# Kernel tuning notes

Hardware: AMD Instinct MI355X
Metric: run time of the kernel (lower is better)

Reference implementation:

```python
import jax, jax.numpy as jnp
import numpy as np

L, N, E, D, H = 3, 20000, 320000, 128, 4
EPS = 1.1920929e-07  # torch RMSNorm default eps = finfo(float32).eps
NEG_SLOPE = 0.2      # PyG GATConv leaky_relu negative_slope


def rmsnorm(x, w):
    return x * jax.lax.rsqrt(jnp.mean(x * x, axis=-1, keepdims=True) + EPS) * w


def setup_inputs() -> dict:
    key = jax.random.key(0)
    ks = jax.random.split(key, 13)
    s = 0.02
    x = jax.random.normal(ks[0], (N, D), jnp.float32)
    src = jax.random.randint(ks[1], (E,), 0, N, dtype=jnp.int64)
    dst = jax.random.randint(ks[2], (E,), 0, N, dtype=jnp.int64)
    dst = jnp.where(dst == src, (dst + 1) % N, dst)  # no pre-existing self loops
    edge_index = jnp.stack([src, dst])
    return {
        "x": x,
        "W_gat": jax.random.normal(ks[3], (L, D, H * D), jnp.float32) * s,
        "att_src": jax.random.normal(ks[4], (L, H, D), jnp.float32) * s,
        "att_dst": jax.random.normal(ks[5], (L, H, D), jnp.float32) * s,
        "bias_gat": jax.random.normal(ks[6], (L, D), jnp.float32) * s,
        "W1": jax.random.normal(ks[7], (L, D, D), jnp.float32) * s,
        "b1": jax.random.normal(ks[8], (L, D), jnp.float32) * s,
        "W2": jax.random.normal(ks[9], (L, D, D), jnp.float32) * s,
        "b2": jax.random.normal(ks[10], (L, D), jnp.float32) * s,
        "norm1_w": jnp.ones((L, D), jnp.float32),
        "norm2_w": jnp.ones((L, D), jnp.float32),
        "edge_index": edge_index,
    }


def reference(x, W_gat, att_src, att_dst, bias_gat, W1, b1, W2, b2, norm1_w, norm2_w, edge_index):
    # PyG GATConv adds self loops by default
    loops = jnp.arange(N, dtype=edge_index.dtype)
    src = jnp.concatenate([edge_index[0], loops])  # [E+N]
    dst = jnp.concatenate([edge_index[1], loops])
    for i in range(L):
        # --- GATConv(hidden, hidden, heads=H, concat=False), dropout=0 (eval) ---
        xp = (x @ W_gat[i]).reshape(N, H, D)               # [N,H,D]
        a_s = jnp.einsum('nhd,hd->nh', xp, att_src[i])     # [N,H]
        a_d = jnp.einsum('nhd,hd->nh', xp, att_dst[i])
        e = jax.nn.leaky_relu(a_s[src] + a_d[dst], NEG_SLOPE)  # [E+N,H]
        m = jax.ops.segment_max(e, dst, num_segments=N)
        ex = jnp.exp(e - m[dst])
        denom = jax.ops.segment_sum(ex, dst, num_segments=N)
        alpha = ex / denom[dst]                             # segment softmax over incoming edges
        agg = jax.ops.segment_sum(alpha[:, :, None] * xp[src], dst, num_segments=N)  # [N,H,D]
        x_att = agg.mean(axis=1) + bias_gat[i]              # concat=False -> head mean, then bias
        # --- residual + RMSNorm ---
        x = rmsnorm(x + x_att, norm1_w[i])
        # --- FFN ---
        h = jax.nn.relu(x @ W1[i] + b1[i])
        h = h @ W2[i] + b2[i]
        x = rmsnorm(x + h, norm2_w[i])
    return x
```

## Files before the change

kernel.cpp:

```cpp
#include <hip/hip_runtime.h>
#include <hip/hip_bf16.h>

#define N_NODES 20000
#define NEDGE   320000
#define DIM     128
#define NH      4
#define HD      512
#define LAYERS  3
#define EPS_RMS 1.1920929e-07f
#define SLOPE   0.2f
#define NTILES  (N_NODES >> 4)

#define NWGC  (LAYERS * DIM * HD)
#define NW1C  (LAYERS * DIM * DIM)
#define NVC   (LAYERS * DIM)
#define NPACK (NWGC + 2 * NW1C + 5 * NVC)
#define NXV   (N_NODES * DIM / 8)

typedef __bf16 bf16_t;
typedef __bf16 bf16v2 __attribute__((ext_vector_type(2)));
typedef __bf16 bf16v8 __attribute__((ext_vector_type(8)));
typedef float  f32v4  __attribute__((ext_vector_type(4)));
typedef float  f32v2  __attribute__((ext_vector_type(2)));

__device__ __forceinline__ int clamp_node(int s) {
    return ((unsigned)s >= (unsigned)N_NODES) ? 0 : s;
}
__device__ __forceinline__ float leaky(float e) { return e > 0.f ? e : SLOPE * e; }
__device__ __forceinline__ unsigned char enc_fp8(float v) {
    int p = __builtin_amdgcn_cvt_pk_fp8_f32(v, v, 0, false);
    return (unsigned char)(p & 0xff);
}
__device__ __forceinline__ unsigned short enc_fp8_pair(float a, float b) {
    int p = __builtin_amdgcn_cvt_pk_fp8_f32(a, b, 0, false);
    return (unsigned short)(p & 0xffff);
}

__device__ __forceinline__ bool wave_detect_bf16(const unsigned short* xh) {
    int lane = threadIdx.x & 63;
    unsigned short hw = xh[2 * lane];
    int e = (hw >> 7) & 0xff;
    unsigned long long b = __ballot(e >= 96 && e <= 140);
    return __popcll(b) >= 48;
}
__device__ __forceinline__ bool wave_detect_i64(const int* ei) {
    int lane = threadIdx.x & 63;
    unsigned long long b = __ballot(ei[2 * lane + 1] != 0);
    return b == 0ULL;
}
__device__ __forceinline__ float raw_elem(const void* in, size_t j, bool isbf) {
    return isbf ? (float)((const bf16_t*)in)[j] : ((const float*)in)[j];
}
__device__ __forceinline__ bf16_t cvt_elem(const void* in, size_t j, bool isbf) {
    return isbf ? ((const bf16_t*)in)[j] : (bf16_t)((const float*)in)[j];
}
__device__ __forceinline__ int edge_src(const int* ei, int e, bool is64) {
    return clamp_node(is64 ? ei[2 * e] : ei[e]);
}
__device__ __forceinline__ int edge_dst(const int* ei, int e, bool is64) {
    return clamp_node(is64 ? ei[2 * NEDGE + 2 * e] : ei[NEDGE + e]);
}

__global__ __launch_bounds__(256) void prep_v(const void* x, const void* Wg,
                                              const void* aS, const void* aD,
                                              float* __restrict__ vS, float* __restrict__ vD,
                                              int* __restrict__ deg) {
    int gid = blockIdx.x * 256 + threadIdx.x;
    for (int i = gid; i < N_NODES; i += gridDim.x * 256) deg[i] = 0;
    bool isbf = wave_detect_bf16((const unsigned short*)x);
    int w = gid >> 6;
    if (w >= LAYERS * DIM * NH * 2) return;
    int lane = threadIdx.x & 63;
    int sd = w & 1, h = (w >> 1) & 3, k = (w >> 3) & 127, l = w >> 10;
    const void* att = sd ? aD : aS;
    size_t wbase = (size_t)l * DIM * HD + (size_t)k * HD + h * DIM;
    size_t abase = (size_t)l * NH * DIM + (size_t)h * DIM;
    int c = 2 * lane;
    float p = raw_elem(Wg, wbase + c, isbf) * raw_elem(att, abase + c, isbf)
            + raw_elem(Wg, wbase + c + 1, isbf) * raw_elem(att, abase + c + 1, isbf);
#pragma unroll
    for (int msk = 1; msk < 64; msk <<= 1) p += __shfl_xor(p, msk);
    if (lane == 0) {
        float* dst = sd ? vD : vS;
        dst[l * HD + h * DIM + k] = p;
    }
}

__device__ __forceinline__ void pack_item(int i, bool isbf,
        const void* Wg, const void* W1, const void* W2,
        const void* bg, const void* b1, const void* b2,
        const void* n1, const void* n2,
        bf16_t* WmixP, bf16_t* W1P, bf16_t* W2P,
        bf16_t* bgc, bf16_t* b1c, bf16_t* b2c, bf16_t* n1c, bf16_t* n2c) {
    if (i < NWGC) {
        int l = i >> 16;
        int r = i & 65535;
        int j = r & 7;
        int lane2 = (r >> 3) & 63;
        int mm = lane2 & 15, kqq = lane2 >> 4;
        int tt = (r >> 9) & 1;
        int kk = (r >> 10) & 15;
        int wvv = r >> 14;
        int kidx = kk * 32 + kqq * 8 + j;
        int h = kidx >> 7, kp = kidx & 127;
        int c = 32 * wvv + tt * 16 + mm;
        WmixP[i] = cvt_elem(Wg, (size_t)l * DIM * HD + (size_t)kp * HD + h * DIM + c, isbf);
        return;
    }
    i -= NWGC;
    if (i < NW1C) {
        int l = i / 16384;
        int r = i & 16383;
        int j = r & 7;
        int lane2 = (r >> 3) & 63;
        int mm = lane2 & 15, kqq = lane2 >> 4;
        int tt = (r >> 9) & 1;
        int ks = (r >> 10) & 3;
        int wvv = r >> 12;
        int k = ks * 32 + kqq * 8 + j;
        int c = 32 * wvv + tt * 16 + mm;
        W1P[i] = cvt_elem(W1, (size_t)l * DIM * DIM + (size_t)k * DIM + c, isbf);
        return;
    }
    i -= NW1C;
    if (i < NW1C) {
        int l = i / 16384;
        int r = i & 16383;
        int j = r & 7;
        int lane2 = (r >> 3) & 63;
        int mm = lane2 & 15, kqq = lane2 >> 4;
        int tt = (r >> 9) & 1;
        int ks = (r >> 10) & 3;
        int wvv = r >> 12;
        int k = ks * 32 + kqq * 8 + j;
        int c = 32 * wvv + tt * 16 + mm;
        W2P[i] = cvt_elem(W2, (size_t)l * DIM * DIM + (size_t)k * DIM + c, isbf);
        return;
    }
    i -= NW1C;
    if (i >= 5 * NVC) return;
    int seg = i / NVC, k = i - seg * NVC;
    if (seg == 0) bgc[k] = cvt_elem(bg, k, isbf);
    else if (seg == 1) b1c[k] = cvt_elem(b1, k, isbf);
    else if (seg == 2) b2c[k] = cvt_elem(b2, k, isbf);
    else if (seg == 3) n1c[k] = cvt_elem(n1, k, isbf);
    else n2c[k] = cvt_elem(n2, k, isbf);
}

__global__ __launch_bounds__(256) void mega_setup(
        const void* x, const void* Wg, const void* W1, const void* W2,
        const void* bg, const void* b1, const void* b2, const void* n1, const void* n2,
        bf16_t* xb, bf16_t* WmixP, bf16_t* W1P, bf16_t* W2P,
        bf16_t* bgc, bf16_t* b1c, bf16_t* b2c, bf16_t* n1c, bf16_t* n2c,
        const int* ei, int* deg,
        const float* vS, const float* vD,
        float* a_s, float* a_d, unsigned short* x8,
        int convBlocks, int histBlocks) {
    int b = (int)blockIdx.x;
    if (b >= convBlocks + histBlocks) {
        bool isbf = wave_detect_bf16((const unsigned short*)x);
        int lane = threadIdx.x & 63;
        int n = (b - convBlocks - histBlocks) * 4 + (int)(threadIdx.x >> 6);
        if (n >= N_NODES) return;
        int c = 2 * lane;
        float f0 = raw_elem(x, (size_t)n * DIM + c, isbf);
        float f1 = raw_elem(x, (size_t)n * DIM + c + 1, isbf);
        x8[n * 64 + lane] = enc_fp8_pair(f0, f1);
#pragma unroll
        for (int h = 0; h < NH; ++h) {
            float ps = f0 * vS[h * DIM + c] + f1 * vS[h * DIM + c + 1];
            float pd = f0 * vD[h * DIM + c] + f1 * vD[h * DIM + c + 1];
#pragma unroll
            for (int msk = 1; msk < 64; msk <<= 1) {
                ps += __shfl_xor(ps, msk);
                pd += __shfl_xor(pd, msk);
            }
            if (lane == 0) {
                a_s[n * 4 + h] = ps;
                a_d[n * 4 + h] = pd;
            }
        }
        return;
    }
    if (b >= convBlocks) {
        bool is64 = wave_detect_i64(ei);
        int e = (b - convBlocks) * 256 + threadIdx.x;
        if (e < NEDGE) atomicAdd(&deg[edge_dst(ei, e, is64)], 1);
        return;
    }
    bool isbf = wave_detect_bf16((const unsigned short*)x);
    int i = b * 256 + threadIdx.x;
    if (i < NXV) {
        if (isbf) {
            ((bf16v8*)xb)[i] = ((const bf16v8*)x)[i];
        } else {
            const float4* src = (const float4*)x;
            float4 a = src[2 * i], bq = src[2 * i + 1];
            bf16v8 o;
            o[0] = (bf16_t)a.x;  o[1] = (bf16_t)a.y;
            o[2] = (bf16_t)a.z;  o[3] = (bf16_t)a.w;
            o[4] = (bf16_t)bq.x; o[5] = (bf16_t)bq.y;
            o[6] = (bf16_t)bq.z; o[7] = (bf16_t)bq.w;
            ((bf16v8*)xb)[i] = o;
        }
        return;
    }
    pack_item(i - NXV, isbf, Wg, W1, W2, bg, b1, b2, n1, n2,
              WmixP, W1P, W2P, bgc, b1c, b2c, n1c, n2c);
}

__global__ __launch_bounds__(1024) void scan_kernel(const int* __restrict__ deg,
                                                    int* __restrict__ row_ptr,
                                                    int* __restrict__ cursor) {
    __shared__ int wsum[16];
    int tid = threadIdx.x, lane = tid & 63, wv = tid >> 6;
    int v[20];
    int base = tid * 20;
    int tot = 0;
    if (base < N_NODES) {
        const int4* d4 = reinterpret_cast<const int4*>(deg + base);
#pragma unroll
        for (int j = 0; j < 5; ++j) {
            int4 q = d4[j];
            v[4 * j]     = q.x;
            v[4 * j + 1] = q.y;
            v[4 * j + 2] = q.z;
            v[4 * j + 3] = q.w;
        }
#pragma unroll
        for (int i = 0; i < 20; ++i) tot += v[i];
    }
    int x = tot;
#pragma unroll
    for (int off = 1; off < 64; off <<= 1) {
        int t = __shfl_up(x, off);
        if (lane >= off) x += t;
    }
    if (lane == 63) wsum[wv] = x;
    __syncthreads();
    if (wv == 0) {
        int s = (lane < 16) ? wsum[lane] : 0;
#pragma unroll
        for (int off = 1; off < 16; off <<= 1) {
            int t = __shfl_up(s, off);
            if (lane >= off) s += t;
        }
        if (lane < 16) wsum[lane] = s;
    }
    __syncthreads();
    int off0 = ((wv == 0) ? 0 : wsum[wv - 1]) + (x - tot);
    if (tid == 0) row_ptr[0] = 0;
    if (base < N_NODES) {
        int run = off0;
#pragma unroll
        for (int i = 0; i < 20; ++i) {
            run += v[i];
            row_ptr[base + i + 1] = run;
            cursor[base + i] = run - v[i];
        }
    }
}

__global__ void fill_kernel(const int* __restrict__ ei, int* __restrict__ cursor,
                            int* __restrict__ csr_src) {
    bool is64 = wave_detect_i64(ei);
    int e = blockIdx.x * blockDim.x + threadIdx.x;
    if (e < NEDGE) {
        int d = edge_dst(ei, e, is64);
        int pos = atomicAdd(&cursor[d], 1);
        if ((unsigned)pos < (unsigned)NEDGE) csr_src[pos] = edge_src(ei, e, is64);
    }
}

__global__ __launch_bounds__(256) void gat_gather(const int* __restrict__ row_ptr,
                                                  const int* __restrict__ csr_src,
                                                  const float* __restrict__ a_s,
                                                  const float* __restrict__ a_d,
                                                  const unsigned short* __restrict__ x8,
                                                  bf16_t* __restrict__ y) {
    __shared__ float4 wsh[4][64];
    __shared__ int    ssh[4][64];
    int n = (int)((blockIdx.x * blockDim.x + threadIdx.x) >> 6);
    if (n >= N_NODES) return;
    int wv = (int)(threadIdx.x >> 6) & 3;
    int lane = threadIdx.x & 63;
    int beg = row_ptr[n];
    int deg = row_ptr[n + 1] - beg;
    if (deg < 0) deg = 0;
    if (deg > NEDGE) deg = NEDGE;
    if (beg < 0) beg = 0;
    if (beg > NEDGE - deg) beg = NEDGE - deg;

    const float4* a_s4 = reinterpret_cast<const float4*>(a_s);
    const float4 adv = reinterpret_cast<const float4*>(a_d)[n];
    const float4 avs = a_s4[n];
    unsigned short pself = x8[n * 64 + lane];
    float4 wself = {__expf(leaky(avs.x + adv.x)), __expf(leaky(avs.y + adv.y)),
                    __expf(leaky(avs.z + adv.z)), __expf(leaky(avs.w + adv.w))};

    float acc[8];
    {
        f32v2 f = __builtin_amdgcn_cvt_pk_f32_fp8((int)pself, false);
        acc[0] = wself.x * f[0]; acc[1] = wself.x * f[1];
        acc[2] = wself.y * f[0]; acc[3] = wself.y * f[1];
        acc[4] = wself.z * f[0]; acc[5] = wself.z * f[1];
        acc[6] = wself.w * f[0]; acc[7] = wself.w * f[1];
    }

    float4 zl = {0.f, 0.f, 0.f, 0.f};
    for (int c0 = 0; c0 < deg; c0 += 64) {
        int cnt = deg - c0; if (cnt > 64) cnt = 64;
        if (lane < cnt) {
            int s = clamp_node(csr_src[beg + c0 + lane]);
            float4 av = a_s4[s];
            float4 w = {__expf(leaky(av.x + adv.x)), __expf(leaky(av.y + adv.y)),
                        __expf(leaky(av.z + adv.z)), __expf(leaky(av.w + adv.w))};
            zl.x += w.x; zl.y += w.y; zl.z += w.z; zl.w += w.w;
            wsh[wv][lane] = w;
            ssh[wv][lane] = s << 6;
        }
        unsigned short xeN[8];
        {
            int p0 = cnt < 8 ? cnt : 8;
#pragma unroll
            for (int u = 0; u < 8; ++u)
                if (u < p0) xeN[u] = x8[ssh[wv][u] + lane];
        }
        for (int u0 = 0; u0 < cnt; u0 += 8) {
            int uc = cnt - u0; if (uc > 8) uc = 8;
            unsigned short xeC[8];
#pragma unroll
            for (int u = 0; u < 8; ++u) xeC[u] = xeN[u];
            int n0 = u0 + 8;
            int nc = cnt - n0; if (nc > 8) nc = 8;
#pragma unroll
            for (int u = 0; u < 8; ++u)
                if (u < nc) xeN[u] = x8[ssh[wv][n0 + u] + lane];
#pragma unroll
            for (int u = 0; u < 8; ++u) {
                if (u < uc) {
                    float4 w = wsh[wv][u0 + u];
                    f32v2 f = __builtin_amdgcn_cvt_pk_f32_fp8((int)xeC[u], false);
                    acc[0] += w.x * f[0]; acc[1] += w.x * f[1];
                    acc[2] += w.y * f[0]; acc[3] += w.y * f[1];
                    acc[4] += w.z * f[0]; acc[5] += w.z * f[1];
                    acc[6] += w.w * f[0]; acc[7] += w.w * f[1];
                }
            }
        }
    }
    float4 zr = zl;
#pragma unroll
    for (int msk = 1; msk < 64; msk <<= 1) {
        zr.x += __shfl_xor(zr.x, msk);
        zr.y += __shfl_xor(zr.y, msk);
        zr.z += __shfl_xor(zr.z, msk);
        zr.w += __shfl_xor(zr.w, msk);
    }
    float4 z4 = {wself.x + zr.x, wself.y + zr.y, wself.z + zr.z, wself.w + zr.w};
    float4 ih4 = {1.f / z4.x, 1.f / z4.y, 1.f / z4.z, 1.f / z4.w};
    int c = 2 * lane;
#pragma unroll
    for (int h = 0; h < NH; ++h) {
        float ih = h == 0 ? ih4.x : h == 1 ? ih4.y : h == 2 ? ih4.z : ih4.w;
        bf16v2 o;
        o[0] = (bf16_t)(acc[h * 2 + 0] * ih);
        o[1] = (bf16_t)(acc[h * 2 + 1] * ih);
        *reinterpret_cast<bf16v2*>(&y[(size_t)n * HD + h * DIM + c]) = o;
    }
}

template <int MODE>
__global__ __launch_bounds__(256) void mix_ffn(
        const bf16_t* __restrict__ y,
        const bf16_t* __restrict__ WmixP, const bf16_t* __restrict__ bg,
        const bf16_t* __restrict__ n1w, const bf16_t* __restrict__ xb,
        const bf16_t* __restrict__ W1P, const bf16_t* __restrict__ b1,
        const bf16_t* __restrict__ W2P, const bf16_t* __restrict__ b2,
        const bf16_t* __restrict__ n2w, void* __restrict__ out,
        const float* __restrict__ vS, const float* __restrict__ vD,
        float* __restrict__ a_s_n, float* __restrict__ a_d_n,
        unsigned char* __restrict__ x8_n) {
    __shared__ bf16_t ylds[16][524];
    __shared__ bf16_t xm[16][140];
    __shared__ float  ssq_p[16][4];
    __shared__ float  asd_p[4][16][8];
    bf16_t (*hh)[140] = reinterpret_cast<bf16_t (*)[140]>(&ylds[0][0]);

    int tile = blockIdx.x;
    int wv = threadIdx.x >> 6;
    int lane = threadIdx.x & 63;
    int m = lane & 15, kq = lane >> 4;

    const bf16_t* ybase = y + (size_t)tile * 16 * HD;
#pragma unroll
    for (int it = 0; it < 8; ++it) {
        int f = it * 2048 + (int)threadIdx.x * 8;
        int row = f >> 9, col = f & 511;
        *reinterpret_cast<bf16v8*>(&ylds[row][col]) =
            *reinterpret_cast<const bf16v8*>(ybase + f);
    }
    __syncthreads();

    f32v4 accm[2];
    accm[0] = (f32v4){0.f, 0.f, 0.f, 0.f};
    accm[1] = (f32v4){0.f, 0.f, 0.f, 0.f};
#pragma unroll
    for (int kk = 0; kk < 16; ++kk) {
        bf16v8 a = *reinterpret_cast<const bf16v8*>(&ylds[m][kk * 32 + kq * 8]);
#pragma unroll
        for (int tt = 0; tt < 2; ++tt) {
            bf16v8 b = *reinterpret_cast<const bf16v8*>(
                WmixP + ((((wv * 16 + kk) * 2 + tt) << 9) + lane * 8));
            accm[tt] = __builtin_amdgcn_mfma_f32_16x16x32_bf16(a, b, accm[tt], 0, 0, 0);
        }
    }
    float vals[2][4];
    {
        float sp[4] = {0.f, 0.f, 0.f, 0.f};
#pragma unroll
        for (int tt = 0; tt < 2; ++tt) {
            int col = 32 * wv + tt * 16 + m;
            float bv = (float)bg[col];
#pragma unroll
            for (int r = 0; r < 4; ++r) {
                int gr = tile * 16 + kq * 4 + r;
                float v = 0.25f * accm[tt][r] + bv + (float)xb[(size_t)gr * DIM + col];
                vals[tt][r] = v;
                sp[r] += v * v;
            }
        }
#pragma unroll
        for (int r = 0; r < 4; ++r) {
            sp[r] += __shfl_xor(sp[r], 1); sp[r] += __shfl_xor(sp[r], 2);
            sp[r] += __shfl_xor(sp[r], 4); sp[r] += __shfl_xor(sp[r], 8);
            if (m == r) ssq_p[kq * 4 + r][wv] = sp[r];
        }
    }
    __syncthreads();
    {
#pragma unroll
        for (int r = 0; r < 4; ++r) {
            int row = kq * 4 + r;
            float s = ssq_p[row][0] + ssq_p[row][1] + ssq_p[row][2] + ssq_p[row][3];
            float scale = rsqrtf(s * (1.f / 128.f) + EPS_RMS);
#pragma unroll
            for (int tt = 0; tt < 2; ++tt) {
                int col = 32 * wv + tt * 16 + m;
                xm[row][col] = (bf16_t)(vals[tt][r] * scale * (float)n1w[col]);
            }
        }
    }
    __syncthreads();

    f32v4 acc1[2];
    acc1[0] = (f32v4){0.f, 0.f, 0.f, 0.f};
    acc1[1] = (f32v4){0.f, 0.f, 0.f, 0.f};
#pragma unroll
    for (int ks = 0; ks < 4; ++ks) {
        bf16v8 a = *reinterpret_cast<const bf16v8*>(&xm[m][ks * 32 + kq * 8]);
#pragma unroll
        for (int tt = 0; tt < 2; ++tt) {
            bf16v8 b = *reinterpret_cast<const bf16v8*>(
                W1P + ((((wv * 4 + ks) * 2 + tt) << 9) + lane * 8));
            acc1[tt] = __builtin_amdgcn_mfma_f32_16x16x32_bf16(a, b, acc1[tt], 0, 0, 0);
        }
    }
#pragma unroll
    for (int tt = 0; tt < 2; ++tt) {
        int col = 32 * wv + tt * 16 + m;
        float bv = (float)b1[col];
#pragma unroll
        for (int r = 0; r < 4; ++r) {
            float v = acc1[tt][r] + bv;
            hh[kq * 4 + r][col] = (bf16_t)(v > 0.f ? v : 0.f);
        }
    }
    __syncthreads();
    f32v4 acc2[2];
    acc2[0] = (f32v4){0.f, 0.f, 0.f, 0.f};
    acc2[1] = (f32v4){0.f, 0.f, 0.f, 0.f};
#pragma unroll
    for (int ks = 0; ks < 4; ++ks) {
        bf16v8 a = *reinterpret_cast<const bf16v8*>(&hh[m][ks * 32 + kq * 8]);
#pragma unroll
        for (int tt = 0; tt < 2; ++tt) {
            bf16v8 b = *reinterpret_cast<const bf16v8*>(
                W2P + ((((wv * 4 + ks) * 2 + tt) << 9) + lane * 8));
            acc2[tt] = __builtin_amdgcn_mfma_f32_16x16x32_bf16(a, b, acc2[tt], 0, 0, 0);
        }
    }
    float vals2[2][4];
    {
        float sp[4] = {0.f, 0.f, 0.f, 0.f};
#pragma unroll
        for (int tt = 0; tt < 2; ++tt) {
            int col = 32 * wv + tt * 16 + m;
            float bv = (float)b2[col];
#pragma unroll
            for (int r = 0; r < 4; ++r) {
                float v = acc2[tt][r] + bv + (float)xm[kq * 4 + r][col];
                vals2[tt][r] = v;
                sp[r] += v * v;
            }
        }
#pragma unroll
        for (int r = 0; r < 4; ++r) {
            sp[r] += __shfl_xor(sp[r], 1); sp[r] += __shfl_xor(sp[r], 2);
            sp[r] += __shfl_xor(sp[r], 4); sp[r] += __shfl_xor(sp[r], 8);
            if (m == r) ssq_p[kq * 4 + r][wv] = sp[r];
        }
    }
    __syncthreads();
    float o2[2][4];
#pragma unroll
    for (int r = 0; r < 4; ++r) {
        int row = kq * 4 + r;
        int gr = tile * 16 + row;
        float s = ssq_p[row][0] + ssq_p[row][1] + ssq_p[row][2] + ssq_p[row][3];
        float scale = rsqrtf(s * (1.f / 128.f) + EPS_RMS);
#pragma unroll
        for (int tt = 0; tt < 2; ++tt) {
            int col = 32 * wv + tt * 16 + m;
            float o = vals2[tt][r] * scale * (float)n2w[col];
            o2[tt][r] = o;
            if (MODE == 1) ((float*)out)[(size_t)gr * DIM + col] = o;
            else {
                ((bf16_t*)out)[(size_t)gr * DIM + col] = (bf16_t)o;
                x8_n[(size_t)gr * DIM + col] = enc_fp8(o);
            }
        }
    }
    if (MODE == 0) {
        float vs0[NH], vs1[NH], vd0[NH], vd1[NH];
        int col0 = 32 * wv + m, col1 = col0 + 16;
#pragma unroll
        for (int h = 0; h < NH; ++h) {
            vs0[h] = vS[h * DIM + col0]; vs1[h] = vS[h * DIM + col1];
            vd0[h] = vD[h * DIM + col0]; vd1[h] = vD[h * DIM + col1];
        }
#pragma unroll
        for (int r = 0; r < 4; ++r) {
#pragma unroll
            for (int h = 0; h < NH; ++h) {
                float ps = o2[0][r] * vs0[h] + o2[1][r] * vs1[h];
                float pd = o2[0][r] * vd0[h] + o2[1][r] * vd1[h];
                ps += __shfl_xor(ps, 1); ps += __shfl_xor(ps, 2);
                ps += __shfl_xor(ps, 4); ps += __shfl_xor(ps, 8);
                pd += __shfl_xor(pd, 1); pd += __shfl_xor(pd, 2);
                pd += __shfl_xor(pd, 4); pd += __shfl_xor(pd, 8);
                if (m == r * 4 + h) {
                    asd_p[wv][kq * 4 + r][h * 2 + 0] = ps;
                    asd_p[wv][kq * 4 + r][h * 2 + 1] = pd;
                }
            }
        }
        __syncthreads();
        int t = threadIdx.x;
        if (t < 128) {
            int row = t >> 3, idx = t & 7;
            float s = asd_p[0][row][idx] + asd_p[1][row][idx]
                    + asd_p[2][row][idx] + asd_p[3][row][idx];
            int gr = tile * 16 + row;
            if (idx & 1) a_d_n[gr * 4 + (idx >> 1)] = s;
            else         a_s_n[gr * 4 + (idx >> 1)] = s;
        }
    }
}

extern "C" void kernel_launch(void* const* d_in, const int* in_sizes, int n_in,
                              void* d_out, int out_size, void* d_ws, size_t ws_size,
                              hipStream_t stream) {
    const void* x_in   = d_in[0];
    const void* W_gat  = d_in[1];
    const void* att_s  = d_in[2];
    const void* att_d  = d_in[3];
    const void* bias_g = d_in[4];
    const void* W1     = d_in[5];
    const void* b1     = d_in[6];
    const void* W2     = d_in[7];
    const void* b2     = d_in[8];
    const void* n1w    = d_in[9];
    const void* n2w    = d_in[10];
    const int*  ei     = (const int*)d_in[11];

    char* ws = (char*)d_ws;
    size_t off = 0;
    auto alloc = [&](size_t bytes) {
        void* p = ws + off;
        off = (off + bytes + 255) & ~(size_t)255;
        return p;
    };
    bf16_t* WmixP   = (bf16_t*)alloc((size_t)LAYERS * HD * DIM * 2);
    bf16_t* W1P     = (bf16_t*)alloc((size_t)LAYERS * DIM * DIM * 2);
    bf16_t* W2P     = (bf16_t*)alloc((size_t)LAYERS * DIM * DIM * 2);
    bf16_t* xb      = (bf16_t*)alloc((size_t)N_NODES * DIM * 2);
    bf16_t* y       = (bf16_t*)alloc((size_t)N_NODES * HD * 2);
    unsigned short* x8a = (unsigned short*)alloc((size_t)N_NODES * DIM);
    unsigned short* x8b = (unsigned short*)alloc((size_t)N_NODES * DIM);
    float*  vS      = (float*)alloc((size_t)LAYERS * HD * 4);
    float*  vD      = (float*)alloc((size_t)LAYERS * HD * 4);
    float*  a_sA    = (float*)alloc((size_t)N_NODES * NH * 4);
    float*  a_dA    = (float*)alloc((size_t)N_NODES * NH * 4);
    float*  a_sB    = (float*)alloc((size_t)N_NODES * NH * 4);
    float*  a_dB    = (float*)alloc((size_t)N_NODES * NH * 4);
    int*    deg     = (int*)alloc((size_t)N_NODES * 4);
    int*    cursor  = (int*)alloc((size_t)N_NODES * 4);
    int*    row_ptr = (int*)alloc((size_t)(N_NODES + 1) * 4);
    int*    csr     = (int*)alloc((size_t)NEDGE * 4);
    bf16_t* bgc     = (bf16_t*)alloc((size_t)LAYERS * DIM * 2);
    bf16_t* b1c     = (bf16_t*)alloc((size_t)LAYERS * DIM * 2);
    bf16_t* b2c     = (bf16_t*)alloc((size_t)LAYERS * DIM * 2);
    bf16_t* n1c     = (bf16_t*)alloc((size_t)LAYERS * DIM * 2);
    bf16_t* n2c     = (bf16_t*)alloc((size_t)LAYERS * DIM * 2);

    prep_v<<<(LAYERS * DIM * NH * 2 * 64 + 255) / 256, 256, 0, stream>>>(
        x_in, W_gat, att_s, att_d, vS, vD, deg);

    const int NTOT = NXV + NPACK;
    const int convBlocks = (NTOT + 255) / 256;
    const int histBlocks = (NEDGE + 255) / 256;
    const int asdBlocks  = (N_NODES + 3) / 4;
    mega_setup<<<convBlocks + histBlocks + asdBlocks, 256, 0, stream>>>(
        x_in, W_gat, W1, W2, bias_g, b1, b2, n1w, n2w,
        xb, WmixP, W1P, W2P, bgc, b1c, b2c, n1c, n2c,
        ei, deg, vS, vD, a_sA, a_dA, x8a, convBlocks, histBlocks);

    scan_kernel<<<1, 1024, 0, stream>>>(deg, row_ptr, cursor);
    fill_kernel<<<(NEDGE + 255) / 256, 256, 0, stream>>>(ei, cursor, csr);

    unsigned short* x8cur[2] = {x8a, x8b};
    float* asCur[2] = {a_sA, a_sB};
    float* adCur[2] = {a_dA, a_dB};
    for (int l = 0; l < LAYERS; ++l) {
        int ci = l & 1, ni = (l + 1) & 1;
        gat_gather<<<(N_NODES * 64 + 255) / 256, 256, 0, stream>>>(
            row_ptr, csr, asCur[ci], adCur[ci], x8cur[ci], y);
        if (l < LAYERS - 1) {
            mix_ffn<0><<<NTILES, 256, 0, stream>>>(
                y, WmixP + (size_t)l * HD * DIM, bgc + (size_t)l * DIM,
                n1c + (size_t)l * DIM, xb,
                W1P + (size_t)l * DIM * DIM, b1c + (size_t)l * DIM,
                W2P + (size_t)l * DIM * DIM, b2c + (size_t)l * DIM,
                n2c + (size_t)l * DIM, xb,
                vS + (size_t)(l + 1) * HD, vD + (size_t)(l + 1) * HD,
                asCur[ni], adCur[ni], (unsigned char*)x8cur[ni]);
        } else {
            mix_ffn<1><<<NTILES, 256, 0, stream>>>(
                y, WmixP + (size_t)l * HD * DIM, bgc + (size_t)l * DIM,
                n1c + (size_t)l * DIM, xb,
                W1P + (size_t)l * DIM * DIM, b1c + (size_t)l * DIM,
                W2P + (size_t)l * DIM * DIM, b2c + (size_t)l * DIM,
                n2c + (size_t)l * DIM, d_out,
                nullptr, nullptr, nullptr, nullptr, nullptr);
        }
    }
}
```

Measured before the change: 301.0 us.

## Fuse GAT neighbor gather into mix/FFN kernel, dropping the y intermediate

The per-node attention gather now runs inside the mix+FFN kernel. Each wave gathers 4 of the tile's 16 nodes and writes the head outputs straight into the shared-memory tile instead of into a global bf16 buffer y. This removes one kernel launch per layer and the global write and read of the N×512 intermediate. The cost is less parallelism: 1250 blocks each handle 16 nodes serially per wave, so latency hiding during the irregular gather may suffer and the LDS footprint grows.

```diff
diff --git a/kernel.cpp b/kernel.cpp
--- a/kernel.cpp
+++ b/kernel.cpp
@@ -272,18 +272,11 @@
     }
 }
 
-__global__ __launch_bounds__(256) void gat_gather(const int* __restrict__ row_ptr,
-                                                  const int* __restrict__ csr_src,
-                                                  const float* __restrict__ a_s,
-                                                  const float* __restrict__ a_d,
-                                                  const unsigned short* __restrict__ x8,
-                                                  bf16_t* __restrict__ y) {
-    __shared__ float4 wsh[4][64];
-    __shared__ int    ssh[4][64];
-    int n = (int)((blockIdx.x * blockDim.x + threadIdx.x) >> 6);
-    if (n >= N_NODES) return;
-    int wv = (int)(threadIdx.x >> 6) & 3;
-    int lane = threadIdx.x & 63;
+__device__ __forceinline__ void gather_node_lds(int n, int lane,
+        float4* wshw, int* sshw,
+        const int* __restrict__ row_ptr, const int* __restrict__ csr_src,
+        const float* __restrict__ a_s, const float* __restrict__ a_d,
+        const unsigned short* __restrict__ x8, bf16_t* yrow) {
     int beg = row_ptr[n];
     int deg = row_ptr[n + 1] - beg;
     if (deg < 0) deg = 0;
@@ -316,15 +309,15 @@
             float4 w = {__expf(leaky(av.x + adv.x)), __expf(leaky(av.y + adv.y)),
                         __expf(leaky(av.z + adv.z)), __expf(leaky(av.w + adv.w))};
             zl.x += w.x; zl.y += w.y; zl.z += w.z; zl.w += w.w;
-            wsh[wv][lane] = w;
-            ssh[wv][lane] = s << 6;
+            wshw[lane] = w;
+            sshw[lane] = s << 6;
         }
         unsigned short xeN[8];
         {
             int p0 = cnt < 8 ? cnt : 8;
 #pragma unroll
             for (int u = 0; u < 8; ++u)
-                if (u < p0) xeN[u] = x8[ssh[wv][u] + lane];
+                if (u < p0) xeN[u] = x8[sshw[u] + lane];
         }
         for (int u0 = 0; u0 < cnt; u0 += 8) {
             int uc = cnt - u0; if (uc > 8) uc = 8;
@@ -335,11 +328,11 @@
             int nc = cnt - n0; if (nc > 8) nc = 8;
 #pragma unroll
             for (int u = 0; u < 8; ++u)
-                if (u < nc) xeN[u] = x8[ssh[wv][n0 + u] + lane];
+                if (u < nc) xeN[u] = x8[sshw[n0 + u] + lane];
 #pragma unroll
             for (int u = 0; u < 8; ++u) {
                 if (u < uc) {
-                    float4 w = wsh[wv][u0 + u];
+                    float4 w = wshw[u0 + u];
                     f32v2 f = __builtin_amdgcn_cvt_pk_f32_fp8((int)xeC[u], false);
                     acc[0] += w.x * f[0]; acc[1] += w.x * f[1];
                     acc[2] += w.y * f[0]; acc[3] += w.y * f[1];
@@ -366,13 +359,15 @@
         bf16v2 o;
         o[0] = (bf16_t)(acc[h * 2 + 0] * ih);
         o[1] = (bf16_t)(acc[h * 2 + 1] * ih);
-        *reinterpret_cast<bf16v2*>(&y[(size_t)n * HD + h * DIM + c]) = o;
+        *reinterpret_cast<bf16v2*>(&yrow[h * DIM + c]) = o;
     }
 }
 
 template <int MODE>
-__global__ __launch_bounds__(256) void mix_ffn(
-        const bf16_t* __restrict__ y,
+__global__ __launch_bounds__(256) void gat_mix(
+        const int* __restrict__ row_ptr, const int* __restrict__ csr_src,
+        const float* __restrict__ a_s, const float* __restrict__ a_d,
+        const unsigned short* __restrict__ x8,
         const bf16_t* __restrict__ WmixP, const bf16_t* __restrict__ bg,
         const bf16_t* __restrict__ n1w, const bf16_t* __restrict__ xb,
         const bf16_t* __restrict__ W1P, const bf16_t* __restrict__ b1,
@@ -385,6 +380,8 @@
     __shared__ bf16_t xm[16][140];
     __shared__ float  ssq_p[16][4];
     __shared__ float  asd_p[4][16][8];
+    __shared__ float4 wsh[4][64];
+    __shared__ int    ssh[4][64];
     bf16_t (*hh)[140] = reinterpret_cast<bf16_t (*)[140]>(&ylds[0][0]);
 
     int tile = blockIdx.x;
@@ -392,14 +389,9 @@
     int lane = threadIdx.x & 63;
     int m = lane & 15, kq = lane >> 4;
 
-    const bf16_t* ybase = y + (size_t)tile * 16 * HD;
-#pragma unroll
-    for (int it = 0; it < 8; ++it) {
-        int f = it * 2048 + (int)threadIdx.x * 8;
-        int row = f >> 9, col = f & 511;
-        *reinterpret_cast<bf16v8*>(&ylds[row][col]) =
-            *reinterpret_cast<const bf16v8*>(ybase + f);
-    }
+    for (int r = wv; r < 16; r += 4)
+        gather_node_lds(tile * 16 + r, lane, wsh[wv], ssh[wv],
+                        row_ptr, csr_src, a_s, a_d, x8, &ylds[r][0]);
     __syncthreads();
 
     f32v4 accm[2];
@@ -595,7 +587,6 @@
     bf16_t* W1P     = (bf16_t*)alloc((size_t)LAYERS * DIM * DIM * 2);
     bf16_t* W2P     = (bf16_t*)alloc((size_t)LAYERS * DIM * DIM * 2);
     bf16_t* xb      = (bf16_t*)alloc((size_t)N_NODES * DIM * 2);
-    bf16_t* y       = (bf16_t*)alloc((size_t)N_NODES * HD * 2);
     unsigned short* x8a = (unsigned short*)alloc((size_t)N_NODES * DIM);
     unsigned short* x8b = (unsigned short*)alloc((size_t)N_NODES * DIM);
     float*  vS      = (float*)alloc((size_t)LAYERS * HD * 4);
@@ -634,11 +625,10 @@
     float* adCur[2] = {a_dA, a_dB};
     for (int l = 0; l < LAYERS; ++l) {
         int ci = l & 1, ni = (l + 1) & 1;
-        gat_gather<<<(N_NODES * 64 + 255) / 256, 256, 0, stream>>>(
-            row_ptr, csr, asCur[ci], adCur[ci], x8cur[ci], y);
         if (l < LAYERS - 1) {
-            mix_ffn<0><<<NTILES, 256, 0, stream>>>(
-                y, WmixP + (size_t)l * HD * DIM, bgc + (size_t)l * DIM,
+            gat_mix<0><<<NTILES, 256, 0, stream>>>(
+                row_ptr, csr, asCur[ci], adCur[ci], x8cur[ci],
+                WmixP + (size_t)l * HD * DIM, bgc + (size_t)l * DIM,
                 n1c + (size_t)l * DIM, xb,
                 W1P + (size_t)l * DIM * DIM, b1c + (size_t)l * DIM,
                 W2P + (size_t)l * DIM * DIM, b2c + (size_t)l * DIM,
@@ -646,8 +636,9 @@
                 vS + (size_t)(l + 1) * HD, vD + (size_t)(l + 1) * HD,
                 asCur[ni], adCur[ni], (unsigned char*)x8cur[ni]);
         } else {
-            mix_ffn<1><<<NTILES, 256, 0, stream>>>(
-                y, WmixP + (size_t)l * HD * DIM, bgc + (size_t)l * DIM,
+            gat_mix<1><<<NTILES, 256, 0, stream>>>(
+                row_ptr, csr, asCur[ci], adCur[ci], x8cur[ci],
+                WmixP + (size_t)l * HD * DIM, bgc + (size_t)l * DIM,
                 n1c + (size_t)l * DIM, xb,
                 W1P + (size_t)l * DIM * DIM, b1c + (size_t)l * DIM,
                 W2P + (size_t)l * DIM * DIM, b2c + (size_t)l * DIM,
```

New measurement: 291.0 us. -3.3%, faster.
